# Performance work log

Hardware: AMD Instinct MI355X
Metric: run time of the kernel (lower is better)

Reference implementation:

```python
import jax, jax.numpy as jnp
import numpy as np

L = 16          # GIF timesteps
BETA = 0.9      # membrane decay
THRESH = 1.0    # firing threshold (soft reset subtracts THRESH)
SG_ALPHA = 4.0  # surrogate-gradient sigmoid sharpness


def setup_inputs() -> dict:
    key = jax.random.key(0)
    k1, k2, k3 = jax.random.split(key, 3)
    B, D_IN, D_H = 65536, 64, 128
    x = jax.random.normal(k1, (B, D_IN), dtype=jnp.float32)
    # Synapsis: Linear(input_dim -> hidden_dim)
    W_syn = jax.random.normal(k2, (D_IN, D_H), dtype=jnp.float32) / np.sqrt(D_IN)
    b_syn = jnp.zeros((D_H,), dtype=jnp.float32)
    # GIFNeuron input projection: Linear(hidden_dim -> hidden_dim)
    W_in = jax.random.normal(k3, (D_H, D_H), dtype=jnp.float32) / np.sqrt(D_H)
    b_in = jnp.zeros((D_H,), dtype=jnp.float32)
    return {"x": x, "W_syn": W_syn, "b_syn": b_syn, "W_in": W_in, "b_in": b_in}


def _spike_fn(v_minus_thresh):
    # Heaviside forward, sigmoid surrogate backward (standard SNN trick).
    sg = jax.nn.sigmoid(SG_ALPHA * v_minus_thresh)
    hard = (v_minus_thresh >= 0.0).astype(v_minus_thresh.dtype)
    return sg + jax.lax.stop_gradient(hard - sg)


def reference(x, W_syn, b_syn, W_in, b_in):
    # Synapsis projection
    h = x @ W_syn + b_syn                      # [B, H]
    # Constant input current to the GIF neuron each timestep
    I = h @ W_in + b_in                        # [B, H]

    def step(carry, _):
        v, s = carry
        v = BETA * v + I - THRESH * s          # leaky integrate + soft reset
        s = _spike_fn(v - THRESH)              # threshold
        return (v, s), s

    v0 = jnp.zeros_like(I)
    s0 = jnp.zeros_like(I)
    (v_final, _), spikes = jax.lax.scan(step, (v0, s0), None, length=L)
    # spikes: [L, B, H], v_final: [B, H]
    return spikes, v_final
```

## Files before the change

kernel.cpp:

```cpp
#include <hip/hip_runtime.h>

#define D_IN 64
#define D_H 128
#define L_STEPS 16
#define ROWS_PER_BLOCK 32
#define THREADS 256

__global__ __launch_bounds__(THREADS) void snn_main(
        const float* __restrict__ x,
        const float* __restrict__ W_syn,
        const float* __restrict__ b_syn,
        const float* __restrict__ W_in,
        const float* __restrict__ b_in,
        float* __restrict__ out,
        int B) {
    __shared__ float xs[ROWS_PER_BLOCK][D_IN];
    __shared__ float hs[ROWS_PER_BLOCK][D_H];

    const int tid = threadIdx.x;
    const long long row0 = (long long)blockIdx.x * ROWS_PER_BLOCK;

    {
        const float4* src = (const float4*)(x + row0 * D_IN);
        float4* dst = (float4*)&xs[0][0];
        dst[tid]       = src[tid];
        dst[tid + 256] = src[tid + 256];
    }
    __syncthreads();

    {
        const int j = tid & 127;
        const int rbase = tid >> 7;
        float wreg[D_IN];
#pragma unroll
        for (int i = 0; i < D_IN; ++i) wreg[i] = W_syn[i * D_H + j];
        const float bs = b_syn[j];
#pragma unroll
        for (int ii = 0; ii < 16; ++ii) {
            const int r = rbase + 2 * ii;
            const float4* xr = (const float4*)&xs[r][0];
            float acc = 0.0f;
#pragma unroll
            for (int i4 = 0; i4 < 16; ++i4) {
                float4 xv = xr[i4];
                acc = __fmaf_rn(xv.x, wreg[4 * i4 + 0], acc);
                acc = __fmaf_rn(xv.y, wreg[4 * i4 + 1], acc);
                acc = __fmaf_rn(xv.z, wreg[4 * i4 + 2], acc);
                acc = __fmaf_rn(xv.w, wreg[4 * i4 + 3], acc);
            }
            hs[r][j] = __fadd_rn(acc, bs);
        }
    }
    __syncthreads();

    const int h0 = (tid & 31) * 4;
    const int rg = (tid >> 5) * 4;

    float acc[4][4];
#pragma unroll
    for (int rr = 0; rr < 4; ++rr)
#pragma unroll
        for (int q = 0; q < 4; ++q) acc[rr][q] = 0.0f;

#pragma unroll 8
    for (int j4 = 0; j4 < 32; ++j4) {
        float hrow[4][4];
#pragma unroll
        for (int rr = 0; rr < 4; ++rr) {
            float4 h4 = *(const float4*)&hs[rg + rr][4 * j4];
            hrow[rr][0] = h4.x; hrow[rr][1] = h4.y;
            hrow[rr][2] = h4.z; hrow[rr][3] = h4.w;
        }
#pragma unroll
        for (int q4 = 0; q4 < 4; ++q4) {
            const int j = 4 * j4 + q4;
            float4 w = *(const float4*)&W_in[j * D_H + h0];
#pragma unroll
            for (int rr = 0; rr < 4; ++rr) {
                const float hv = hrow[rr][q4];
                acc[rr][0] = __fmaf_rn(hv, w.x, acc[rr][0]);
                acc[rr][1] = __fmaf_rn(hv, w.y, acc[rr][1]);
                acc[rr][2] = __fmaf_rn(hv, w.z, acc[rr][2]);
                acc[rr][3] = __fmaf_rn(hv, w.w, acc[rr][3]);
            }
        }
    }

    const float4 bi = *(const float4*)&b_in[h0];
    float Iv[4][4];
#pragma unroll
    for (int rr = 0; rr < 4; ++rr) {
        Iv[rr][0] = __fadd_rn(acc[rr][0], bi.x);
        Iv[rr][1] = __fadd_rn(acc[rr][1], bi.y);
        Iv[rr][2] = __fadd_rn(acc[rr][2], bi.z);
        Iv[rr][3] = __fadd_rn(acc[rr][3], bi.w);
    }

    const size_t BH = (size_t)B * D_H;
    float* __restrict__ vout = out + (size_t)L_STEPS * BH;

#pragma unroll
    for (int rr = 0; rr < 4; ++rr) {
        const size_t base = (size_t)(row0 + rg + rr) * D_H + (size_t)h0;
        float v0 = 0.f, v1 = 0.f, v2 = 0.f, v3 = 0.f;
        float s0 = 0.f, s1 = 0.f, s2 = 0.f, s3 = 0.f;
        const float I0 = Iv[rr][0], I1 = Iv[rr][1], I2 = Iv[rr][2], I3 = Iv[rr][3];
#pragma unroll
        for (int t = 0; t < L_STEPS; ++t) {
            v0 = __fsub_rn(__fadd_rn(__fmul_rn(0.9f, v0), I0), s0);
            v1 = __fsub_rn(__fadd_rn(__fmul_rn(0.9f, v1), I1), s1);
            v2 = __fsub_rn(__fadd_rn(__fmul_rn(0.9f, v2), I2), s2);
            v3 = __fsub_rn(__fadd_rn(__fmul_rn(0.9f, v3), I3), s3);
            s0 = (v0 >= 1.0f) ? 1.0f : 0.0f;
            s1 = (v1 >= 1.0f) ? 1.0f : 0.0f;
            s2 = (v2 >= 1.0f) ? 1.0f : 0.0f;
            s3 = (v3 >= 1.0f) ? 1.0f : 0.0f;
            float4 s4 = make_float4(s0, s1, s2, s3);
            *(float4*)(out + (size_t)t * BH + base) = s4;
        }
        float4 v4 = make_float4(v0, v1, v2, v3);
        *(float4*)(vout + base) = v4;
    }
}

extern "C" void kernel_launch(void* const* d_in, const int* in_sizes, int n_in,
                              void* d_out, int out_size, void* d_ws, size_t ws_size,
                              hipStream_t stream) {
    const float* x     = (const float*)d_in[0];
    const float* W_syn = (const float*)d_in[1];
    const float* b_syn = (const float*)d_in[2];
    const float* W_in  = (const float*)d_in[3];
    const float* b_in  = (const float*)d_in[4];
    float* out = (float*)d_out;

    const int B = in_sizes[0] / D_IN;

    snn_main<<<dim3(B / ROWS_PER_BLOCK), dim3(THREADS), 0, stream>>>(
        x, W_syn, b_syn, W_in, b_in, out, B);
}
```

Baseline: 675.7 us.

## Split GEMM and spike recurrence into two kernels with nontemporal stores

Splits the fused kernel in two. The first kernel computes the input current I and writes it to a workspace buffer. The second is a grid-stride kernel that reads I and runs the 16-step recurrence, writing spikes and the final voltage with nontemporal stores. The aim is to decouple the compute-heavy GEMM from the store-bound output phase so each can saturate its resource and avoid cache pollution. In exchange it adds a 32 MB write and read of I plus a second launch.

```diff
diff --git a/kernel.cpp b/kernel.cpp
--- a/kernel.cpp
+++ b/kernel.cpp
@@ -6,13 +6,15 @@
 #define ROWS_PER_BLOCK 32
 #define THREADS 256
 
-__global__ __launch_bounds__(THREADS) void snn_main(
+typedef float f32x4 __attribute__((ext_vector_type(4)));
+
+__global__ __launch_bounds__(THREADS) void snn_gemm(
         const float* __restrict__ x,
         const float* __restrict__ W_syn,
         const float* __restrict__ b_syn,
         const float* __restrict__ W_in,
         const float* __restrict__ b_in,
-        float* __restrict__ out,
+        float* __restrict__ I_out,
         int B) {
     __shared__ float xs[ROWS_PER_BLOCK][D_IN];
     __shared__ float hs[ROWS_PER_BLOCK][D_H];
@@ -87,24 +89,32 @@
     }
 
     const float4 bi = *(const float4*)&b_in[h0];
-    float Iv[4][4];
 #pragma unroll
     for (int rr = 0; rr < 4; ++rr) {
-        Iv[rr][0] = __fadd_rn(acc[rr][0], bi.x);
-        Iv[rr][1] = __fadd_rn(acc[rr][1], bi.y);
-        Iv[rr][2] = __fadd_rn(acc[rr][2], bi.z);
-        Iv[rr][3] = __fadd_rn(acc[rr][3], bi.w);
+        float4 Iv;
+        Iv.x = __fadd_rn(acc[rr][0], bi.x);
+        Iv.y = __fadd_rn(acc[rr][1], bi.y);
+        Iv.z = __fadd_rn(acc[rr][2], bi.z);
+        Iv.w = __fadd_rn(acc[rr][3], bi.w);
+        *(float4*)(I_out + (size_t)(row0 + rg + rr) * D_H + (size_t)h0) = Iv;
     }
+}
 
+__global__ __launch_bounds__(256) void snn_recur(
+        const float* __restrict__ I,
+        float* __restrict__ out,
+        int B) {
     const size_t BH = (size_t)B * D_H;
+    const size_t nquads = BH >> 2;
+    const size_t stride = (size_t)gridDim.x * 256u;
     float* __restrict__ vout = out + (size_t)L_STEPS * BH;
 
-#pragma unroll
-    for (int rr = 0; rr < 4; ++rr) {
-        const size_t base = (size_t)(row0 + rg + rr) * D_H + (size_t)h0;
+    for (size_t q = (size_t)blockIdx.x * 256u + threadIdx.x; q < nquads; q += stride) {
+        const f32x4 I4 = ((const f32x4*)I)[q];
+        const float I0 = I4.x, I1 = I4.y, I2 = I4.z, I3 = I4.w;
         float v0 = 0.f, v1 = 0.f, v2 = 0.f, v3 = 0.f;
         float s0 = 0.f, s1 = 0.f, s2 = 0.f, s3 = 0.f;
-        const float I0 = Iv[rr][0], I1 = Iv[rr][1], I2 = Iv[rr][2], I3 = Iv[rr][3];
+        float* base = out + 4 * q;
 #pragma unroll
         for (int t = 0; t < L_STEPS; ++t) {
             v0 = __fsub_rn(__fadd_rn(__fmul_rn(0.9f, v0), I0), s0);
@@ -115,11 +125,11 @@
             s1 = (v1 >= 1.0f) ? 1.0f : 0.0f;
             s2 = (v2 >= 1.0f) ? 1.0f : 0.0f;
             s3 = (v3 >= 1.0f) ? 1.0f : 0.0f;
-            float4 s4 = make_float4(s0, s1, s2, s3);
-            *(float4*)(out + (size_t)t * BH + base) = s4;
+            f32x4 s4 = {s0, s1, s2, s3};
+            __builtin_nontemporal_store(s4, (f32x4*)(base + (size_t)t * BH));
         }
-        float4 v4 = make_float4(v0, v1, v2, v3);
-        *(float4*)(vout + base) = v4;
+        f32x4 v4 = {v0, v1, v2, v3};
+        __builtin_nontemporal_store(v4, (f32x4*)(vout + 4 * q));
     }
 }
 
@@ -134,7 +144,10 @@
     float* out = (float*)d_out;
 
     const int B = in_sizes[0] / D_IN;
+    float* I = (float*)d_ws;
 
-    snn_main<<<dim3(B / ROWS_PER_BLOCK), dim3(THREADS), 0, stream>>>(
-        x, W_syn, b_syn, W_in, b_in, out, B);
+    snn_gemm<<<dim3(B / ROWS_PER_BLOCK), dim3(THREADS), 0, stream>>>(
+        x, W_syn, b_syn, W_in, b_in, I, B);
+
+    snn_recur<<<dim3(2048), dim3(256), 0, stream>>>(I, out, B);
 }
```

New measurement: 637.2 us. 5.7% less time.
